# Kernel optimization log

Hardware: AMD Instinct MI355X
Metric: run time of the kernel (lower is better)

The kernel has to match this reference:

```python
import jax, jax.numpy as jnp
import numpy as np
import jax.scipy.linalg as jsl

T = 2048      # number of time steps
N = 8192      # number of particles / states
D = 4         # matrix_size (dims[-1] = 16)
H = 128       # MLP hidden width

def setup_inputs() -> dict:
    key = jax.random.key(0)
    ks = jax.random.split(key, 8)
    x = jax.random.normal(ks[0], (N, D), dtype=jnp.float32)
    t = jnp.sort(jax.random.uniform(ks[1], (T,), dtype=jnp.float32))
    # MLP params, stored (in, out); torch Linear does x @ W.T + b
    def xavier(k, fan_in, fan_out):
        s = jnp.sqrt(2.0 / (fan_in + fan_out))
        return (s * jax.random.normal(k, (fan_in, fan_out))).astype(jnp.float32)
    W1 = xavier(ks[2], 1, H); b1 = jnp.zeros((H,), jnp.float32)
    W2 = xavier(ks[3], H, H); b2 = jnp.zeros((H,), jnp.float32)
    W3 = xavier(ks[4], H, D * D); b3 = jnp.zeros((D * D,), jnp.float32)
    M0 = jnp.zeros((D, D), jnp.float32)  # zero buffer (M0=None)
    return {"x": x, "t": t, "M0": M0, "W1": W1, "b1": b1,
            "W2": W2, "b2": b2, "W3": W3, "b3": b3}

def reference(x, t, M0, W1, b1, W2, b2, W3, b3):
    t0 = 0.0
    tt = jnp.concatenate([jnp.full((1, 1), t0, t.dtype), t.reshape(-1, 1)], axis=0)  # (T+1,1)
    delta_t = tt[1:] - tt[:-1]          # (T,1)
    t_avg = (tt[1:] + tt[:-1]) * 0.5    # (T,1)
    # per-step MLP -> (T, D*D)
    h = jnp.tanh(t_avg @ W1 + b1)
    h = jnp.tanh(h @ W2 + b2)
    A = (h @ W3 + b3).reshape(-1, D, D)
    A = A + M0[None, :, :]
    A = A * delta_t[:, :, None]         # (T,D,D) scaled by dt
    # lie_algebra = identity
    A_sum = jnp.cumsum(A, axis=0)       # prefix-sum over time
    E = jax.vmap(jsl.expm)(A_sum)       # batched matrix exponential (T,D,D)
    out = jnp.einsum('tij,nj->tni', E, x)  # (T,N,D)
    return out
```

## Files before the change

### kernel.cpp

```cpp
#include <hip/hip_runtime.h>
#include <math.h>

#define TT 2048
#define NN 8192
#define DD 4
#define HH 128

__global__ void mlp_kernel(const float* __restrict__ t_arr,
                           const float* __restrict__ M0,
                           const float* __restrict__ W1, const float* __restrict__ b1,
                           const float* __restrict__ W2, const float* __restrict__ b2,
                           const float* __restrict__ W3, const float* __restrict__ b3,
                           float* __restrict__ A_t) {
    const int t = blockIdx.x;
    const int j = threadIdx.x;
    __shared__ float h1[HH];
    __shared__ float h2[HH];

    const float t_cur  = t_arr[t];
    const float t_prev = (t > 0) ? t_arr[t - 1] : 0.0f;
    const float dt = t_cur - t_prev;
    const float ta = 0.5f * (t_cur + t_prev);

    h1[j] = tanhf(fmaf(ta, W1[j], b1[j]));
    __syncthreads();

    float acc = b2[j];
    #pragma unroll 8
    for (int i = 0; i < HH; ++i) acc = fmaf(h1[i], W2[i * HH + j], acc);
    h2[j] = tanhf(acc);
    __syncthreads();

    if (j < 16) {
        float a = b3[j];
        #pragma unroll 8
        for (int i = 0; i < HH; ++i) a = fmaf(h2[i], W3[i * 16 + j], a);
        a = (a + M0[j]) * dt;
        A_t[j * TT + t] = a;
    }
}

__global__ void scan_kernel(const float* __restrict__ A_t, float* __restrict__ Asum) {
    const int tid = threadIdx.x;
    const int e = tid >> 6;
    const int c = tid & 63;
    const float* src = A_t + e * TT + c * 32;

    float v[32];
    float s = 0.0f;
    #pragma unroll
    for (int i = 0; i < 32; ++i) { v[i] = src[i]; s += v[i]; }

    __shared__ float cs[16 * 64];
    cs[e * 64 + c] = s;
    __syncthreads();

    if (c == 0) {
        float run = 0.0f;
        const int base = e * 64;
        for (int i = 0; i < 64; ++i) {
            const float x = cs[base + i];
            cs[base + i] = run;
            run += x;
        }
    }
    __syncthreads();

    float run = cs[e * 64 + c];
    const int t0 = c * 32;
    #pragma unroll
    for (int i = 0; i < 32; ++i) {
        run += v[i];
        Asum[(t0 + i) * 16 + e] = run;
    }
}

__device__ __forceinline__ void mm4(const float* __restrict__ A,
                                    const float* __restrict__ B,
                                    float* __restrict__ C) {
    #pragma unroll
    for (int i = 0; i < 4; ++i) {
        #pragma unroll
        for (int j = 0; j < 4; ++j) {
            float s = 0.0f;
            #pragma unroll
            for (int k = 0; k < 4; ++k) s = fmaf(A[i * 4 + k], B[k * 4 + j], s);
            C[i * 4 + j] = s;
        }
    }
}

__global__ void expm_kernel(const float* __restrict__ Asum, float* __restrict__ E) {
    const int t = blockIdx.x * blockDim.x + threadIdx.x;
    if (t >= TT) return;

    float M[16];
    const float4* src = (const float4*)(Asum + t * 16);
    #pragma unroll
    for (int r = 0; r < 4; ++r) {
        float4 v = src[r];
        M[r * 4 + 0] = v.x; M[r * 4 + 1] = v.y; M[r * 4 + 2] = v.z; M[r * 4 + 3] = v.w;
    }

    float nrm = 0.0f;
    #pragma unroll
    for (int i = 0; i < 4; ++i) {
        float rs = fabsf(M[i*4+0]) + fabsf(M[i*4+1]) + fabsf(M[i*4+2]) + fabsf(M[i*4+3]);
        nrm = fmaxf(nrm, rs);
    }
    int k = 0;
    while (nrm > 0.5f && k < 40) { nrm *= 0.5f; ++k; }
    const float sc = ldexpf(1.0f, -k);
    #pragma unroll
    for (int i = 0; i < 16; ++i) M[i] *= sc;

    float R[16], P[16], Q[16];
    #pragma unroll
    for (int i = 0; i < 16; ++i) { P[i] = M[i]; R[i] = M[i]; }
    R[0] += 1.0f; R[5] += 1.0f; R[10] += 1.0f; R[15] += 1.0f;
    for (int n = 2; n <= 12; ++n) {
        mm4(P, M, Q);
        const float inv = 1.0f / (float)n;
        #pragma unroll
        for (int i = 0; i < 16; ++i) { P[i] = Q[i] * inv; R[i] += P[i]; }
    }
    for (int s = 0; s < k; ++s) {
        mm4(R, R, Q);
        #pragma unroll
        for (int i = 0; i < 16; ++i) R[i] = Q[i];
    }

    float4* dst = (float4*)(E + t * 16);
    #pragma unroll
    for (int r = 0; r < 4; ++r)
        dst[r] = make_float4(R[r*4+0], R[r*4+1], R[r*4+2], R[r*4+3]);
}

__global__ void apply_kernel(const float* __restrict__ E,
                             const float* __restrict__ x,
                             float* __restrict__ out) {
    const int t = blockIdx.y;
    const int n = blockIdx.x * blockDim.x + threadIdx.x;

    __shared__ float Es[16];
    if (threadIdx.x < 16) Es[threadIdx.x] = E[t * 16 + threadIdx.x];
    __syncthreads();

    const float4 xv = ((const float4*)x)[n];
    float4 o;
    o.x = fmaf(Es[0],  xv.x, fmaf(Es[1],  xv.y, fmaf(Es[2],  xv.z, Es[3]  * xv.w)));
    o.y = fmaf(Es[4],  xv.x, fmaf(Es[5],  xv.y, fmaf(Es[6],  xv.z, Es[7]  * xv.w)));
    o.z = fmaf(Es[8],  xv.x, fmaf(Es[9],  xv.y, fmaf(Es[10], xv.z, Es[11] * xv.w)));
    o.w = fmaf(Es[12], xv.x, fmaf(Es[13], xv.y, fmaf(Es[14], xv.z, Es[15] * xv.w)));

    ((float4*)out)[(size_t)t * NN + n] = o;
}

extern "C" void kernel_launch(void* const* d_in, const int* in_sizes, int n_in,
                              void* d_out, int out_size, void* d_ws, size_t ws_size,
                              hipStream_t stream) {
    const float* x  = (const float*)d_in[0];
    const float* t  = (const float*)d_in[1];
    const float* M0 = (const float*)d_in[2];
    const float* W1 = (const float*)d_in[3];
    const float* b1 = (const float*)d_in[4];
    const float* W2 = (const float*)d_in[5];
    const float* b2 = (const float*)d_in[6];
    const float* W3 = (const float*)d_in[7];
    const float* b3 = (const float*)d_in[8];
    float* out = (float*)d_out;

    float* A_t  = (float*)d_ws;
    float* Asum = A_t  + 16 * TT;
    float* E    = Asum + 16 * TT;

    mlp_kernel<<<TT, HH, 0, stream>>>(t, M0, W1, b1, W2, b2, W3, b3, A_t);
    scan_kernel<<<1, 1024, 0, stream>>>(A_t, Asum);
    expm_kernel<<<TT / 256, 256, 0, stream>>>(Asum, E);
    apply_kernel<<<dim3(NN / 256, TT), 256, 0, stream>>>(E, x, out);
}
```

Baseline: 306.5 us.

## Batch MLP timesteps, fuse scan with expm, and use nontemporal stores in apply

The MLP kernel now handles four timesteps per block, so each W2/W3 weight load is reused across four accumulators. The scan and matrix-exponential kernels are merged into one single-block launch, which removes a kernel launch. The apply kernel reads E straight into registers instead of going through shared memory, processes four float4 elements per thread, and writes the output with nontemporal stores. The output write of 268MB dominates the runtime, so the main gain is expected from the store path. The fused expm now runs in one block of 1024 threads rather than eight blocks, which may serialize that stage.

```diff
diff --git a/kernel.cpp b/kernel.cpp
--- a/kernel.cpp
+++ b/kernel.cpp
@@ -3,44 +3,80 @@
 
 #define TT 2048
 #define NN 8192
-#define DD 4
 #define HH 128
-
-__global__ void mlp_kernel(const float* __restrict__ t_arr,
-                           const float* __restrict__ M0,
-                           const float* __restrict__ W1, const float* __restrict__ b1,
-                           const float* __restrict__ W2, const float* __restrict__ b2,
-                           const float* __restrict__ W3, const float* __restrict__ b3,
-                           float* __restrict__ A_t) {
-    const int t = blockIdx.x;
+#define TPB 4
+
+typedef float f4 __attribute__((ext_vector_type(4)));
+
+__global__ __launch_bounds__(HH) void mlp_kernel(
+        const float* __restrict__ t_arr, const float* __restrict__ M0,
+        const float* __restrict__ W1, const float* __restrict__ b1,
+        const float* __restrict__ W2, const float* __restrict__ b2,
+        const float* __restrict__ W3, const float* __restrict__ b3,
+        float* __restrict__ A_t) {
+    const int tb = blockIdx.x * TPB;
     const int j = threadIdx.x;
-    __shared__ float h1[HH];
-    __shared__ float h2[HH];
-
-    const float t_cur  = t_arr[t];
-    const float t_prev = (t > 0) ? t_arr[t - 1] : 0.0f;
-    const float dt = t_cur - t_prev;
-    const float ta = 0.5f * (t_cur + t_prev);
-
-    h1[j] = tanhf(fmaf(ta, W1[j], b1[j]));
-    __syncthreads();
-
-    float acc = b2[j];
-    #pragma unroll 8
-    for (int i = 0; i < HH; ++i) acc = fmaf(h1[i], W2[i * HH + j], acc);
-    h2[j] = tanhf(acc);
+    __shared__ float h1[TPB][HH];
+    __shared__ float h2[TPB][HH];
+    __shared__ float dts[TPB];
+
+    #pragma unroll
+    for (int q = 0; q < TPB; ++q) {
+        const int t = tb + q;
+        const float t_cur  = t_arr[t];
+        const float t_prev = (t > 0) ? t_arr[t - 1] : 0.0f;
+        if (j == 0) dts[q] = t_cur - t_prev;
+        const float ta = 0.5f * (t_cur + t_prev);
+        h1[q][j] = tanhf(fmaf(ta, W1[j], b1[j]));
+    }
+    __syncthreads();
+
+    float acc[TPB];
+    #pragma unroll
+    for (int q = 0; q < TPB; ++q) acc[q] = b2[j];
+    #pragma unroll 4
+    for (int i = 0; i < HH; ++i) {
+        const float w = W2[i * HH + j];
+        #pragma unroll
+        for (int q = 0; q < TPB; ++q) acc[q] = fmaf(h1[q][i], w, acc[q]);
+    }
+    #pragma unroll
+    for (int q = 0; q < TPB; ++q) h2[q][j] = tanhf(acc[q]);
     __syncthreads();
 
     if (j < 16) {
-        float a = b3[j];
-        #pragma unroll 8
-        for (int i = 0; i < HH; ++i) a = fmaf(h2[i], W3[i * 16 + j], a);
-        a = (a + M0[j]) * dt;
-        A_t[j * TT + t] = a;
-    }
-}
-
-__global__ void scan_kernel(const float* __restrict__ A_t, float* __restrict__ Asum) {
+        float a[TPB];
+        #pragma unroll
+        for (int q = 0; q < TPB; ++q) a[q] = b3[j];
+        #pragma unroll 4
+        for (int i = 0; i < HH; ++i) {
+            const float w = W3[i * 16 + j];
+            #pragma unroll
+            for (int q = 0; q < TPB; ++q) a[q] = fmaf(h2[q][i], w, a[q]);
+        }
+        #pragma unroll
+        for (int q = 0; q < TPB; ++q)
+            A_t[j * TT + tb + q] = (a[q] + M0[j]) * dts[q];
+    }
+}
+
+__device__ __forceinline__ void mm4(const float* __restrict__ A,
+                                    const float* __restrict__ B,
+                                    float* __restrict__ C) {
+    #pragma unroll
+    for (int i = 0; i < 4; ++i)
+        #pragma unroll
+        for (int j = 0; j < 4; ++j) {
+            float s = 0.0f;
+            #pragma unroll
+            for (int k = 0; k < 4; ++k) s = fmaf(A[i * 4 + k], B[k * 4 + j], s);
+            C[i * 4 + j] = s;
+        }
+}
+
+__global__ __launch_bounds__(1024) void scan_expm_kernel(
+        const float* __restrict__ A_t, float* __restrict__ Asum,
+        float* __restrict__ E) {
     const int tid = threadIdx.x;
     const int e = tid >> 6;
     const int c = tid & 63;
@@ -59,9 +95,9 @@
         float run = 0.0f;
         const int base = e * 64;
         for (int i = 0; i < 64; ++i) {
-            const float x = cs[base + i];
+            const float xv = cs[base + i];
             cs[base + i] = run;
-            run += x;
+            run += xv;
         }
     }
     __syncthreads();
@@ -73,87 +109,78 @@
         run += v[i];
         Asum[(t0 + i) * 16 + e] = run;
     }
-}
-
-__device__ __forceinline__ void mm4(const float* __restrict__ A,
-                                    const float* __restrict__ B,
-                                    float* __restrict__ C) {
-    #pragma unroll
-    for (int i = 0; i < 4; ++i) {
-        #pragma unroll
-        for (int j = 0; j < 4; ++j) {
-            float s = 0.0f;
-            #pragma unroll
-            for (int k = 0; k < 4; ++k) s = fmaf(A[i * 4 + k], B[k * 4 + j], s);
-            C[i * 4 + j] = s;
-        }
-    }
-}
-
-__global__ void expm_kernel(const float* __restrict__ Asum, float* __restrict__ E) {
-    const int t = blockIdx.x * blockDim.x + threadIdx.x;
-    if (t >= TT) return;
-
-    float M[16];
-    const float4* src = (const float4*)(Asum + t * 16);
-    #pragma unroll
-    for (int r = 0; r < 4; ++r) {
-        float4 v = src[r];
-        M[r * 4 + 0] = v.x; M[r * 4 + 1] = v.y; M[r * 4 + 2] = v.z; M[r * 4 + 3] = v.w;
-    }
-
-    float nrm = 0.0f;
-    #pragma unroll
-    for (int i = 0; i < 4; ++i) {
-        float rs = fabsf(M[i*4+0]) + fabsf(M[i*4+1]) + fabsf(M[i*4+2]) + fabsf(M[i*4+3]);
-        nrm = fmaxf(nrm, rs);
-    }
-    int k = 0;
-    while (nrm > 0.5f && k < 40) { nrm *= 0.5f; ++k; }
-    const float sc = ldexpf(1.0f, -k);
-    #pragma unroll
-    for (int i = 0; i < 16; ++i) M[i] *= sc;
-
-    float R[16], P[16], Q[16];
-    #pragma unroll
-    for (int i = 0; i < 16; ++i) { P[i] = M[i]; R[i] = M[i]; }
-    R[0] += 1.0f; R[5] += 1.0f; R[10] += 1.0f; R[15] += 1.0f;
-    for (int n = 2; n <= 12; ++n) {
-        mm4(P, M, Q);
-        const float inv = 1.0f / (float)n;
-        #pragma unroll
-        for (int i = 0; i < 16; ++i) { P[i] = Q[i] * inv; R[i] += P[i]; }
-    }
-    for (int s = 0; s < k; ++s) {
-        mm4(R, R, Q);
-        #pragma unroll
-        for (int i = 0; i < 16; ++i) R[i] = Q[i];
-    }
-
-    float4* dst = (float4*)(E + t * 16);
-    #pragma unroll
-    for (int r = 0; r < 4; ++r)
-        dst[r] = make_float4(R[r*4+0], R[r*4+1], R[r*4+2], R[r*4+3]);
-}
-
-__global__ void apply_kernel(const float* __restrict__ E,
-                             const float* __restrict__ x,
-                             float* __restrict__ out) {
+    __threadfence_block();
+    __syncthreads();
+
+    for (int t = tid; t < TT; t += 1024) {
+        float M[16];
+        const f4* ms = (const f4*)(Asum + t * 16);
+        #pragma unroll
+        for (int r = 0; r < 4; ++r) {
+            f4 vv = ms[r];
+            M[r*4+0] = vv.x; M[r*4+1] = vv.y; M[r*4+2] = vv.z; M[r*4+3] = vv.w;
+        }
+        float nrm = 0.0f;
+        #pragma unroll
+        for (int i = 0; i < 4; ++i) {
+            float rs = fabsf(M[i*4+0]) + fabsf(M[i*4+1]) + fabsf(M[i*4+2]) + fabsf(M[i*4+3]);
+            nrm = fmaxf(nrm, rs);
+        }
+        int k = 0;
+        while (nrm > 0.5f && k < 40) { nrm *= 0.5f; ++k; }
+        const float sc = ldexpf(1.0f, -k);
+        #pragma unroll
+        for (int i = 0; i < 16; ++i) M[i] *= sc;
+
+        float R[16], P[16], Q[16];
+        #pragma unroll
+        for (int i = 0; i < 16; ++i) { P[i] = M[i]; R[i] = M[i]; }
+        R[0] += 1.0f; R[5] += 1.0f; R[10] += 1.0f; R[15] += 1.0f;
+        for (int n = 2; n <= 12; ++n) {
+            mm4(P, M, Q);
+            const float inv = 1.0f / (float)n;
+            #pragma unroll
+            for (int i = 0; i < 16; ++i) { P[i] = Q[i] * inv; R[i] += P[i]; }
+        }
+        for (int sq = 0; sq < k; ++sq) {
+            mm4(R, R, Q);
+            #pragma unroll
+            for (int i = 0; i < 16; ++i) R[i] = Q[i];
+        }
+        f4* dst = (f4*)(E + t * 16);
+        #pragma unroll
+        for (int r = 0; r < 4; ++r) {
+            f4 o; o.x = R[r*4+0]; o.y = R[r*4+1]; o.z = R[r*4+2]; o.w = R[r*4+3];
+            dst[r] = o;
+        }
+    }
+}
+
+__global__ __launch_bounds__(256) void apply_kernel(
+        const float* __restrict__ E, const float* __restrict__ x,
+        float* __restrict__ out) {
     const int t = blockIdx.y;
-    const int n = blockIdx.x * blockDim.x + threadIdx.x;
-
-    __shared__ float Es[16];
-    if (threadIdx.x < 16) Es[threadIdx.x] = E[t * 16 + threadIdx.x];
-    __syncthreads();
-
-    const float4 xv = ((const float4*)x)[n];
-    float4 o;
-    o.x = fmaf(Es[0],  xv.x, fmaf(Es[1],  xv.y, fmaf(Es[2],  xv.z, Es[3]  * xv.w)));
-    o.y = fmaf(Es[4],  xv.x, fmaf(Es[5],  xv.y, fmaf(Es[6],  xv.z, Es[7]  * xv.w)));
-    o.z = fmaf(Es[8],  xv.x, fmaf(Es[9],  xv.y, fmaf(Es[10], xv.z, Es[11] * xv.w)));
-    o.w = fmaf(Es[12], xv.x, fmaf(Es[13], xv.y, fmaf(Es[14], xv.z, Es[15] * xv.w)));
-
-    ((float4*)out)[(size_t)t * NN + n] = o;
+    const float* __restrict__ Ep = E + t * 16;
+    const float e0 = Ep[0],  e1 = Ep[1],  e2 = Ep[2],  e3 = Ep[3];
+    const float e4 = Ep[4],  e5 = Ep[5],  e6 = Ep[6],  e7 = Ep[7];
+    const float e8 = Ep[8],  e9 = Ep[9],  e10 = Ep[10], e11 = Ep[11];
+    const float e12 = Ep[12], e13 = Ep[13], e14 = Ep[14], e15 = Ep[15];
+
+    const f4* __restrict__ x4 = (const f4*)x;
+    f4* __restrict__ o4 = (f4*)out + (size_t)t * NN;
+    const int base = blockIdx.x * 1024 + threadIdx.x;
+
+    #pragma unroll
+    for (int k = 0; k < 4; ++k) {
+        const int n = base + k * 256;
+        const f4 xv = x4[n];
+        f4 o;
+        o.x = fmaf(e0,  xv.x, fmaf(e1,  xv.y, fmaf(e2,  xv.z, e3  * xv.w)));
+        o.y = fmaf(e4,  xv.x, fmaf(e5,  xv.y, fmaf(e6,  xv.z, e7  * xv.w)));
+        o.z = fmaf(e8,  xv.x, fmaf(e9,  xv.y, fmaf(e10, xv.z, e11 * xv.w)));
+        o.w = fmaf(e12, xv.x, fmaf(e13, xv.y, fmaf(e14, xv.z, e15 * xv.w)));
+        __builtin_nontemporal_store(o, &o4[n]);
+    }
 }
 
 extern "C" void kernel_launch(void* const* d_in, const int* in_sizes, int n_in,
@@ -174,8 +201,7 @@
     float* Asum = A_t  + 16 * TT;
     float* E    = Asum + 16 * TT;
 
-    mlp_kernel<<<TT, HH, 0, stream>>>(t, M0, W1, b1, W2, b2, W3, b3, A_t);
-    scan_kernel<<<1, 1024, 0, stream>>>(A_t, Asum);
-    expm_kernel<<<TT / 256, 256, 0, stream>>>(Asum, E);
-    apply_kernel<<<dim3(NN / 256, TT), 256, 0, stream>>>(E, x, out);
-}
+    mlp_kernel<<<TT / TPB, HH, 0, stream>>>(t, M0, W1, b1, W2, b2, W3, b3, A_t);
+    scan_expm_kernel<<<1, 1024, 0, stream>>>(A_t, Asum, E);
+    apply_kernel<<<dim3(NN / 1024, TT), 256, 0, stream>>>(E, x, out);
+}
```

Measured after the change: 340.7 us. +11.2%, slower.
